# Performance work log

Measured on AMD Instinct MI355X. Metric: run time of the kernel, lower is better.

## Reference

```python
import jax, jax.numpy as jnp
import numpy as np

N_HEADS = 16
THETA = 10000.0


def _rope_cos_sin(seq_len, head_dim):
    # freqs_cis = exp(i * pos * theta^(-2j/d)), shape (seq_len, head_dim//2)
    inv_freq = 1.0 / (THETA ** (np.arange(0, head_dim, 2, dtype=np.float32) / head_dim))
    ang = np.arange(seq_len, dtype=np.float32)[:, None] * inv_freq[None, :]
    return jnp.asarray(np.cos(ang)), jnp.asarray(np.sin(ang))


def _apply_rope(t, cos, sin):
    # t: [B, S, H, hd]; rotate consecutive pairs as complex numbers
    B, S, H, hd = t.shape
    pairs = t.reshape(B, S, H, hd // 2, 2)
    r, i = pairs[..., 0], pairs[..., 1]
    c = cos[None, :, None, :]  # [1, S, 1, hd//2]
    s = sin[None, :, None, :]
    out_r = r * c - i * s
    out_i = r * s + i * c
    return jnp.stack([out_r, out_i], axis=-1).reshape(B, S, H, hd)


def setup_inputs() -> dict:
    key = jax.random.key(0)
    ks = jax.random.split(key, 5)
    B, S, D = 2, 2048, 2048
    scale = 1.0 / np.sqrt(D)
    return {
        "x": jax.random.normal(ks[0], (B, S, D), dtype=jnp.float32),
        "wq": jax.random.normal(ks[1], (D, D), dtype=jnp.float32) * scale,
        "wk": jax.random.normal(ks[2], (D, D), dtype=jnp.float32) * scale,
        "wv": jax.random.normal(ks[3], (D, D), dtype=jnp.float32) * scale,
        "wo": jax.random.normal(ks[4], (D, D), dtype=jnp.float32) * scale,
    }


def reference(x, wq, wk, wv, wo):
    B, S, D = x.shape
    H = N_HEADS
    hd = D // H
    cos, sin = _rope_cos_sin(S, hd)

    xq = (x @ wq.T).reshape(B, S, H, hd)
    xk = (x @ wk.T).reshape(B, S, H, hd)
    xv = (x @ wv.T).reshape(B, S, H, hd)

    xq = _apply_rope(xq, cos, sin)
    xk = _apply_rope(xk, cos, sin)

    # [B, H, S, S] scores, full (non-causal) softmax as in the source
    scores = jnp.einsum("bqhd,bkhd->bhqk", xq, xk) / jnp.sqrt(jnp.float32(hd))
    attn = jax.nn.softmax(scores, axis=-1)
    out = jnp.einsum("bhqk,bkhd->bqhd", attn, xv).reshape(B, S, D)
    return out @ wo.T
```

## Files before the change

kernel.cpp:

```cpp
#include <hip/hip_runtime.h>
#include <hip/hip_bf16.h>
#include <stdint.h>


typedef __attribute__((ext_vector_type(4))) float f32x4;
typedef __attribute__((ext_vector_type(8))) short bf16x8;

typedef __attribute__((address_space(3))) unsigned int lds_u32;
typedef __attribute__((address_space(1))) const unsigned int gbl_u32;

__device__ __forceinline__ void async16(const void* g, void* l) {
  __builtin_amdgcn_global_load_lds((gbl_u32*)g, (lds_u32*)l, 16, 0, 0);
}

__device__ __forceinline__ float bf_to_f(unsigned short u) {
  union { unsigned int i; float f; } v; v.i = ((unsigned int)u) << 16; return v.f;
}
__device__ __forceinline__ unsigned short f_to_bf(float f) {
  union { float f; unsigned int i; } v; v.f = f;
  unsigned int r = v.i + 0x7FFFu + ((v.i >> 16) & 1u);
  return (unsigned short)(r >> 16);
}
__device__ __forceinline__ unsigned int cvt_pk_bf16(float lo, float hi) {
  unsigned int r;
  asm("v_cvt_pk_bf16_f32 %0, %1, %2" : "=v"(r) : "v"(lo), "v"(hi));
  return r;
}

#define B_ 2
#define S_ 2048
#define D_ 2048
#define H_ 16
#define HD_ 128

__global__ __launch_bounds__(256) void conv_all(const float* __restrict__ x,
                                                const float* __restrict__ wq,
                                                const float* __restrict__ wk,
                                                const float* __restrict__ wv,
                                                const float* __restrict__ wo,
                                                unsigned short* __restrict__ xb,
                                                unsigned short* __restrict__ wb) {
  int i = blockIdx.x * 256 + threadIdx.x;
  const float* s;
  unsigned short* d;
  int off;
  if (i < 2097152) {
    s = x; d = xb; off = i;
  } else {
    int j = i - 2097152;
    int t = j >> 20;
    off = j & 1048575;
    s = (t == 0) ? wq : (t == 1) ? wk : (t == 2) ? wv : wo;
    d = wb + (size_t)t * 4194304;
  }
  float4 v = ((const float4*)s)[off];
  uint2 o;
  o.x = (unsigned int)f_to_bf(v.x) | ((unsigned int)f_to_bf(v.y) << 16);
  o.y = (unsigned int)f_to_bf(v.z) | ((unsigned int)f_to_bf(v.w) << 16);
  ((uint2*)d)[off] = o;
}

__global__ __launch_bounds__(256) void rope_table_kernel(float* __restrict__ cosT,
                                                         float* __restrict__ sinT) {
  int i = blockIdx.x * 256 + threadIdx.x;
  int s = i >> 6, j = i & 63;
  float inv = powf(10000.0f, -(float)(2 * j) * (1.0f / 128.0f));
  float ang = (float)s * inv;
  float sv, cv;
  sincosf(ang, &sv, &cv);
  cosT[i] = cv;
  sinT[i] = sv;
}

template <int MODE>
__global__ __launch_bounds__(256, 3) void gemm_bt(const unsigned short* __restrict__ A,
                                                  const unsigned short* __restrict__ Bm,
                                                  unsigned short* __restrict__ Cb,
                                                  float* __restrict__ Cf,
                                                  const float* __restrict__ cosT,
                                                  const float* __restrict__ sinT,
                                                  int M, int N, int K) {
  __shared__ unsigned short sA[128 * 32];
  __shared__ unsigned short sB[128 * 32];
  const int tid = threadIdx.x;
  const int l = tid & 63, wv = tid >> 6;
  const int lane15 = l & 15, lhi = l >> 4;
  const int wm = wv >> 1, wn = wv & 1;
  const int bm = blockIdx.x, bn = blockIdx.y;
  const unsigned short* Ag = A + (size_t)bm * 128 * K;
  const unsigned short* Bg = Bm + (size_t)bn * 128 * K;

  f32x4 acc[4][4];
  const f32x4 zero = {0.f, 0.f, 0.f, 0.f};
#pragma unroll
  for (int i = 0; i < 4; i++)
#pragma unroll
    for (int j = 0; j < 4; j++) acc[i][j] = zero;

  for (int k0 = 0; k0 < K; k0 += 32) {
    __syncthreads();
#pragma unroll
    for (int i = 0; i < 2; i++) {
      int c = i * 256 + tid;
      int row = c >> 2, col = (c & 3) << 3;
      async16(Ag + (size_t)row * K + k0 + col, &sA[c * 8]);
      async16(Bg + (size_t)row * K + k0 + col, &sB[c * 8]);
    }
    __syncthreads();

    bf16x8 af[4], bfr[4];
#pragma unroll
    for (int i = 0; i < 4; i++)
      af[i] = *(const bf16x8*)&sA[(wm * 64 + i * 16 + lane15) * 32 + lhi * 8];
#pragma unroll
    for (int j = 0; j < 4; j++)
      bfr[j] = *(const bf16x8*)&sB[(wn * 64 + j * 16 + lane15) * 32 + lhi * 8];
#pragma unroll
    for (int i = 0; i < 4; i++)
#pragma unroll
      for (int j = 0; j < 4; j++)
        acc[i][j] = __builtin_amdgcn_mfma_f32_16x16x32_bf16(af[i], bfr[j], acc[i][j], 0, 0, 0);
  }

#pragma unroll
  for (int i = 0; i < 4; i++) {
    int m0 = bm * 128 + wm * 64 + i * 16 + lhi * 4;
#pragma unroll
    for (int j = 0; j < 4; j++) {
      int n = bn * 128 + wn * 64 + j * 16 + lane15;
      if constexpr (MODE == 0) {
#pragma unroll
        for (int r = 0; r < 4; r++) Cb[(size_t)(m0 + r) * N + n] = f_to_bf(acc[i][j][r]);
      } else if constexpr (MODE == 1) {
#pragma unroll
        for (int r = 0; r < 4; r++) Cf[(size_t)(m0 + r) * N + n] = acc[i][j][r];
      } else if constexpr (MODE == 2) {
        int s0 = m0 & (S_ - 1);
        int jp = (n & (HD_ - 1)) >> 1;
        int odd = n & 1;
#pragma unroll
        for (int r = 0; r < 4; r++) {
          float own = acc[i][j][r];
          float prt = __shfl_xor(own, 1);
          float c = cosT[(s0 + r) * 64 + jp];
          float sn = sinT[(s0 + r) * 64 + jp];
          float outv = odd ? fmaf(prt, sn, own * c) : own * c - prt * sn;
          Cb[(size_t)(m0 + r) * N + n] = f_to_bf(outv);
        }
      } else {
        int s0 = m0 & (S_ - 1);
        size_t row = (size_t)((m0 >> 11) * D_ + n);
        uint2 st;
        st.x = (unsigned int)f_to_bf(acc[i][j][0]) | ((unsigned int)f_to_bf(acc[i][j][1]) << 16);
        st.y = (unsigned int)f_to_bf(acc[i][j][2]) | ((unsigned int)f_to_bf(acc[i][j][3]) << 16);
        *(uint2*)(Cb + row * S_ + s0) = st;
      }
    }
  }
}

__global__ __launch_bounds__(512, 2) void attn_kernel(const unsigned short* __restrict__ Q,
                                                      const unsigned short* __restrict__ K,
                                                      const unsigned short* __restrict__ Vt,
                                                      unsigned short* __restrict__ ctx,
                                                      const float* __restrict__ cosT,
                                                      const float* __restrict__ sinT) {
  __shared__ unsigned short sK[2][64 * 128];
  __shared__ unsigned short sV[2][128 * 64];
  __shared__ unsigned short sP[8][32 * 72];
  const int tid = threadIdx.x, l = tid & 63, w = tid >> 6;
  const int lane15 = l & 15, lhi = l >> 4;
  const int bh = blockIdx.x * 4 + (blockIdx.y >> 3);
  const int qt = blockIdx.y & 7;
  const int b = bh >> 4, h = bh & 15;
  const int q0 = qt * 256;
  const unsigned short* Kg = K + ((size_t)(b * S_)) * D_ + h * HD_;
  const unsigned short* Vg = Vt + ((size_t)bh * HD_) * S_;
  const float qscale = 0.08838834764831845f * 1.44269504f;
  const float THR = 11.5415603f;

  const unsigned short* gp0;
  const unsigned short* gp1;
  const unsigned short* gp2;
  const unsigned short* gp3;
  unsigned int ldsOff[4];
  int gstride;
  if (w < 4) {
    const unsigned short* t0;
#pragma unroll
    for (int i = 0; i < 4; i++) {
      int row = w * 16 + i * 4 + (l >> 4);
      int colD = (l & 15) << 4;
      int colS = colD ^ ((row & 7) << 4);
      t0 = Kg + (size_t)row * D_ + (colS >> 1);
      if (i == 0) gp0 = t0; else if (i == 1) gp1 = t0; else if (i == 2) gp2 = t0; else gp3 = t0;
      ldsOff[i] = row * 256 + colD;
    }
    gstride = 64 * D_;
  } else {
    const unsigned short* t0;
#pragma unroll
    for (int i = 0; i < 4; i++) {
      int row = (w - 4) * 32 + i * 8 + (l >> 3);
      int colD = (l & 7) << 4;
      int colS = colD ^ ((row & 7) << 4);
      t0 = Vg + (size_t)row * S_ + (colS >> 1);
      if (i == 0) gp0 = t0; else if (i == 1) gp1 = t0; else if (i == 2) gp2 = t0; else gp3 = t0;
      ldsOff[i] = row * 128 + colD;
    }
    gstride = 64;
  }

  bf16x8 qf[2][4];
#pragma unroll
  for (int s = 0; s < 2; s++) {
    int s_q = q0 + w * 32 + s * 16 + lane15;
    const unsigned short* Qrow = Q + ((size_t)(b * S_ + s_q)) * D_ + h * HD_;
#pragma unroll
    for (int kc = 0; kc < 4; kc++) {
      int d0 = kc * 32 + lhi * 8;
      uint4 raw = *(const uint4*)(Qrow + d0);
      float4 cv = *(const float4*)(cosT + (size_t)s_q * 64 + (d0 >> 1));
      float4 sv = *(const float4*)(sinT + (size_t)s_q * 64 + (d0 >> 1));
      unsigned int u[4] = {raw.x, raw.y, raw.z, raw.w};
      float cc[4] = {cv.x, cv.y, cv.z, cv.w};
      float ss[4] = {sv.x, sv.y, sv.z, sv.w};
      unsigned int o[4];
#pragma unroll
      for (int p = 0; p < 4; p++) {
        float re = bf_to_f((unsigned short)(u[p] & 0xffffu));
        float im = bf_to_f((unsigned short)(u[p] >> 16));
        float orr = (re * cc[p] - im * ss[p]) * qscale;
        float oi = (re * ss[p] + im * cc[p]) * qscale;
        o[p] = (unsigned int)f_to_bf(orr) | ((unsigned int)f_to_bf(oi) << 16);
      }
      union { uint4 u4; bf16x8 v; } cvt;
      cvt.u4.x = o[0]; cvt.u4.y = o[1]; cvt.u4.z = o[2]; cvt.u4.w = o[3];
      qf[s][kc] = cvt.v;
    }
  }

  float mrun[2] = {-1e30f, -1e30f}, lrun[2] = {0.f, 0.f};
  const f32x4 zero = {0.f, 0.f, 0.f, 0.f};
  f32x4 oacc[2][8];
#pragma unroll
  for (int s = 0; s < 2; s++)
#pragma unroll
    for (int nf = 0; nf < 8; nf++) oacc[s][nf] = zero;

  {
    char* base = (w < 4) ? (char*)&sK[0][0] : (char*)&sV[0][0];
    async16(gp0, base + ldsOff[0]);
    async16(gp1, base + ldsOff[1]);
    async16(gp2, base + ldsOff[2]);
    async16(gp3, base + ldsOff[3]);
    gp0 += gstride; gp1 += gstride; gp2 += gstride; gp3 += gstride;
  }

  for (int t = 0; t < 32; ++t) {
    const int cur = t & 1;
    __syncthreads();
    if (t < 31) {
      char* base = (w < 4) ? (char*)&sK[cur ^ 1][0] : (char*)&sV[cur ^ 1][0];
      async16(gp0, base + ldsOff[0]);
      async16(gp1, base + ldsOff[1]);
      async16(gp2, base + ldsOff[2]);
      async16(gp3, base + ldsOff[3]);
      gp0 += gstride; gp1 += gstride; gp2 += gstride; gp3 += gstride;
    }
    const unsigned short* sKc = sK[cur];
    const unsigned short* sVc = sV[cur];

    f32x4 sacc[2][4];
#pragma unroll
    for (int s = 0; s < 2; s++)
#pragma unroll
      for (int n = 0; n < 4; n++) sacc[s][n] = zero;
    __builtin_amdgcn_s_setprio(1);
#pragma unroll
    for (int n = 0; n < 4; n++) {
      int row = n * 16 + lane15;
#pragma unroll
      for (int kc = 0; kc < 4; kc++) {
        bf16x8 kf = *(const bf16x8*)((const char*)sKc + row * 256 +
                                     ((kc * 64 + lhi * 16) ^ ((row & 7) << 4)));
        sacc[0][n] = __builtin_amdgcn_mfma_f32_16x16x32_bf16(kf, qf[0][kc], sacc[0][n], 0, 0, 0);
        sacc[1][n] = __builtin_amdgcn_mfma_f32_16x16x32_bf16(kf, qf[1][kc], sacc[1][n], 0, 0, 0);
      }
    }
    __builtin_amdgcn_s_setprio(0);

    float pmax[2];
#pragma unroll
    for (int s = 0; s < 2; s++) {
      float a0 = fmaxf(fmaxf(sacc[s][0][0], sacc[s][0][1]), fmaxf(sacc[s][0][2], sacc[s][0][3]));
      float a1 = fmaxf(fmaxf(sacc[s][1][0], sacc[s][1][1]), fmaxf(sacc[s][1][2], sacc[s][1][3]));
      float a2 = fmaxf(fmaxf(sacc[s][2][0], sacc[s][2][1]), fmaxf(sacc[s][2][2], sacc[s][2][3]));
      float a3 = fmaxf(fmaxf(sacc[s][3][0], sacc[s][3][1]), fmaxf(sacc[s][3][2], sacc[s][3][3]));
      float pm = fmaxf(fmaxf(a0, a1), fmaxf(a2, a3));
      pm = fmaxf(pm, __shfl_xor(pm, 16));
      pm = fmaxf(pm, __shfl_xor(pm, 32));
      pmax[s] = pm;
    }
    if (!__all(fmaxf(pmax[0] - mrun[0], pmax[1] - mrun[1]) <= THR)) {
#pragma unroll
      for (int s = 0; s < 2; s++) {
        float mnew = fmaxf(mrun[s], pmax[s]);
        float alpha = exp2f(mrun[s] - mnew);
        lrun[s] *= alpha;
        float af[4];
#pragma unroll
        for (int r = 0; r < 4; r++) af[r] = __shfl(alpha, lhi * 4 + r);
#pragma unroll
        for (int nf = 0; nf < 8; nf++)
#pragma unroll
          for (int r = 0; r < 4; r++) oacc[s][nf][r] *= af[r];
        mrun[s] = mnew;
      }
    }
#pragma unroll
    for (int s = 0; s < 2; s++) {
      float rs = 0.f;
      float p[4][4];
#pragma unroll
      for (int n = 0; n < 4; n++)
#pragma unroll
        for (int r = 0; r < 4; r++) {
          float pv = exp2f(sacc[s][n][r] - mrun[s]);
          p[n][r] = pv;
          rs += pv;
        }
      rs += __shfl_xor(rs, 16);
      rs += __shfl_xor(rs, 32);
      lrun[s] += rs;
#pragma unroll
      for (int n = 0; n < 4; n++) {
        uint2 st;
        st.x = cvt_pk_bf16(p[n][0], p[n][1]);
        st.y = cvt_pk_bf16(p[n][2], p[n][3]);
        *(uint2*)&sP[w][(s * 16 + lane15) * 72 + n * 16 + lhi * 4] = st;
      }
    }
    asm volatile("s_waitcnt lgkmcnt(0)" ::: "memory");
    __builtin_amdgcn_sched_barrier(0);
    bf16x8 pf[2][2];
#pragma unroll
    for (int s = 0; s < 2; s++)
#pragma unroll
      for (int kc = 0; kc < 2; kc++)
        pf[s][kc] = *(const bf16x8*)&sP[w][(s * 16 + lane15) * 72 + kc * 32 + lhi * 8];

    __builtin_amdgcn_s_setprio(1);
#pragma unroll
    for (int nf = 0; nf < 8; nf++) {
      int row = nf * 16 + lane15;
#pragma unroll
      for (int kc = 0; kc < 2; kc++) {
        bf16x8 vf = *(const bf16x8*)((const char*)sVc + row * 128 +
                                     ((kc * 64 + lhi * 16) ^ ((row & 7) << 4)));
        oacc[0][nf] = __builtin_amdgcn_mfma_f32_16x16x32_bf16(pf[0][kc], vf, oacc[0][nf], 0, 0, 0);
        oacc[1][nf] = __builtin_amdgcn_mfma_f32_16x16x32_bf16(pf[1][kc], vf, oacc[1][nf], 0, 0, 0);
      }
    }
    __builtin_amdgcn_s_setprio(0);
  }

#pragma unroll
  for (int s = 0; s < 2; s++) {
    float inv = 1.0f / lrun[s];
    float invr[4];
#pragma unroll
    for (int r = 0; r < 4; r++) invr[r] = __shfl(inv, lhi * 4 + r);
    unsigned short* Og = ctx + ((size_t)(b * S_ + q0 + w * 32 + s * 16)) * D_ + h * HD_;
#pragma unroll
    for (int r = 0; r < 4; r++) {
      int qrow = lhi * 4 + r;
#pragma unroll
      for (int nf = 0; nf < 8; nf++)
        Og[(size_t)qrow * D_ + nf * 16 + lane15] = f_to_bf(oacc[s][nf][r] * invr[r]);
    }
  }
}

extern "C" void kernel_launch(void* const* d_in, const int* in_sizes, int n_in,
                              void* d_out, int out_size, void* d_ws, size_t ws_size,
                              hipStream_t stream) {
  (void)in_sizes; (void)n_in; (void)out_size; (void)ws_size;
  const float* x = (const float*)d_in[0];
  const float* wq = (const float*)d_in[1];
  const float* wk = (const float*)d_in[2];
  const float* wv = (const float*)d_in[3];
  const float* wo = (const float*)d_in[4];
  float* out = (float*)d_out;

  char* ws = (char*)d_ws;
  const size_t MB = 1024 * 1024;
  unsigned short* xb  = (unsigned short*)(ws + 0 * MB);
  unsigned short* wqb = (unsigned short*)(ws + 16 * MB);
  unsigned short* wkb = (unsigned short*)(ws + 24 * MB);
  unsigned short* wvb = (unsigned short*)(ws + 32 * MB);
  unsigned short* wob = (unsigned short*)(ws + 40 * MB);
  unsigned short* Qb  = (unsigned short*)(ws + 48 * MB);
  unsigned short* Kb  = (unsigned short*)(ws + 64 * MB);
  unsigned short* Vtb = (unsigned short*)(ws + 80 * MB);
  float* cosT = (float*)(ws + 96 * MB);
  float* sinT = (float*)(ws + 96 * MB + 524288);
  unsigned short* ctxb = xb;

  const int M = B_ * S_;

  conv_all<<<24576, 256, 0, stream>>>(x, wq, wk, wv, wo, xb, wqb);
  rope_table_kernel<<<512, 256, 0, stream>>>(cosT, sinT);

  dim3 ggrid(M / 128, D_ / 128);
  gemm_bt<0><<<ggrid, 256, 0, stream>>>(xb, wqb, Qb, nullptr, nullptr, nullptr, M, D_, D_);
  gemm_bt<2><<<ggrid, 256, 0, stream>>>(xb, wkb, Kb, nullptr, cosT, sinT, M, D_, D_);
  gemm_bt<3><<<ggrid, 256, 0, stream>>>(xb, wvb, Vtb, nullptr, nullptr, nullptr, M, D_, D_);

  attn_kernel<<<dim3(8, 32), 512, 0, stream>>>(Qb, Kb, Vtb, ctxb, cosT, sinT);

  gemm_bt<1><<<ggrid, 256, 0, stream>>>(ctxb, wob, nullptr, out, nullptr, nullptr, M, D_, D_);
}
```

Before: 314.6 us.

## Shrink attention blocks to 4 waves, swap P via permlane, remap grid per XCD

The attention kernel now runs 256-thread blocks of 128 query rows each, launched as a 1D grid of 512 blocks. Block indices are mapped so that the blocks sharing one batch-head land on the same XCD, which should improve L2 reuse of K and V. Every wave now loads both K and V tiles, where before half the waves loaded each. The P matrix goes from the C-fragment layout to the A-operand layout with v_permlane32/16_swap in registers rather than a round trip through LDS, which removes the sP buffer, its LDS traffic and the waitcnt. In exchange each block issues more loads per wave and there are twice as many blocks.

Result: no change. 320.7 us (+1.9%).

```diff
diff --git a/kernel.cpp b/kernel.cpp
--- a/kernel.cpp
+++ b/kernel.cpp
@@ -159,7 +159,7 @@
   }
 }
 
-__global__ __launch_bounds__(512, 2) void attn_kernel(const unsigned short* __restrict__ Q,
+__global__ __launch_bounds__(256, 2) void attn_kernel(const unsigned short* __restrict__ Q,
                                                       const unsigned short* __restrict__ K,
                                                       const unsigned short* __restrict__ Vt,
                                                       unsigned short* __restrict__ ctx,
@@ -167,48 +167,34 @@
                                                       const float* __restrict__ sinT) {
   __shared__ unsigned short sK[2][64 * 128];
   __shared__ unsigned short sV[2][128 * 64];
-  __shared__ unsigned short sP[8][32 * 72];
   const int tid = threadIdx.x, l = tid & 63, w = tid >> 6;
   const int lane15 = l & 15, lhi = l >> 4;
-  const int bh = blockIdx.x * 4 + (blockIdx.y >> 3);
-  const int qt = blockIdx.y & 7;
+  const int wg = blockIdx.x;
+  const int xcd = wg & 7, rest = wg >> 3;
+  const int bh = xcd * 4 + (rest >> 4);
+  const int qt = rest & 15;
   const int b = bh >> 4, h = bh & 15;
-  const int q0 = qt * 256;
+  const int q0 = qt * 128;
   const unsigned short* Kg = K + ((size_t)(b * S_)) * D_ + h * HD_;
   const unsigned short* Vg = Vt + ((size_t)bh * HD_) * S_;
   const float qscale = 0.08838834764831845f * 1.44269504f;
   const float THR = 11.5415603f;
 
-  const unsigned short* gp0;
-  const unsigned short* gp1;
-  const unsigned short* gp2;
-  const unsigned short* gp3;
-  unsigned int ldsOff[4];
-  int gstride;
-  if (w < 4) {
-    const unsigned short* t0;
-#pragma unroll
-    for (int i = 0; i < 4; i++) {
-      int row = w * 16 + i * 4 + (l >> 4);
-      int colD = (l & 15) << 4;
-      int colS = colD ^ ((row & 7) << 4);
-      t0 = Kg + (size_t)row * D_ + (colS >> 1);
-      if (i == 0) gp0 = t0; else if (i == 1) gp1 = t0; else if (i == 2) gp2 = t0; else gp3 = t0;
-      ldsOff[i] = row * 256 + colD;
-    }
-    gstride = 64 * D_;
-  } else {
-    const unsigned short* t0;
-#pragma unroll
-    for (int i = 0; i < 4; i++) {
-      int row = (w - 4) * 32 + i * 8 + (l >> 3);
-      int colD = (l & 7) << 4;
-      int colS = colD ^ ((row & 7) << 4);
-      t0 = Vg + (size_t)row * S_ + (colS >> 1);
-      if (i == 0) gp0 = t0; else if (i == 1) gp1 = t0; else if (i == 2) gp2 = t0; else gp3 = t0;
-      ldsOff[i] = row * 128 + colD;
-    }
-    gstride = 64;
+  const unsigned short* gpK[4];
+  const unsigned short* gpV[4];
+  unsigned int offK[4], offV[4];
+#pragma unroll
+  for (int i = 0; i < 4; i++) {
+    int rowK = w * 16 + i * 4 + (l >> 4);
+    int cDK = (l & 15) << 4;
+    int cSK = cDK ^ ((rowK & 7) << 4);
+    gpK[i] = Kg + (size_t)rowK * D_ + (cSK >> 1);
+    offK[i] = rowK * 256 + cDK;
+    int rowV = w * 32 + i * 8 + (l >> 3);
+    int cDV = (l & 7) << 4;
+    int cSV = cDV ^ ((rowV & 7) << 4);
+    gpV[i] = Vg + (size_t)rowV * S_ + (cSV >> 1);
+    offV[i] = rowV * 128 + cDV;
   }
 
   bf16x8 qf[2][4];
@@ -248,25 +234,31 @@
 #pragma unroll
     for (int nf = 0; nf < 8; nf++) oacc[s][nf] = zero;
 
-  {
-    char* base = (w < 4) ? (char*)&sK[0][0] : (char*)&sV[0][0];
-    async16(gp0, base + ldsOff[0]);
-    async16(gp1, base + ldsOff[1]);
-    async16(gp2, base + ldsOff[2]);
-    async16(gp3, base + ldsOff[3]);
-    gp0 += gstride; gp1 += gstride; gp2 += gstride; gp3 += gstride;
+#pragma unroll
+  for (int i = 0; i < 4; i++) {
+    async16(gpK[i], (char*)&sK[0][0] + offK[i]);
+    gpK[i] += 64 * D_;
+  }
+#pragma unroll
+  for (int i = 0; i < 4; i++) {
+    async16(gpV[i], (char*)&sV[0][0] + offV[i]);
+    gpV[i] += 64;
   }
 
   for (int t = 0; t < 32; ++t) {
     const int cur = t & 1;
     __syncthreads();
     if (t < 31) {
-      char* base = (w < 4) ? (char*)&sK[cur ^ 1][0] : (char*)&sV[cur ^ 1][0];
-      async16(gp0, base + ldsOff[0]);
-      async16(gp1, base + ldsOff[1]);
-      async16(gp2, base + ldsOff[2]);
-      async16(gp3, base + ldsOff[3]);
-      gp0 += gstride; gp1 += gstride; gp2 += gstride; gp3 += gstride;
+#pragma unroll
+      for (int i = 0; i < 4; i++) {
+        async16(gpK[i], (char*)&sK[cur ^ 1][0] + offK[i]);
+        gpK[i] += 64 * D_;
+      }
+#pragma unroll
+      for (int i = 0; i < 4; i++) {
+        async16(gpV[i], (char*)&sV[cur ^ 1][0] + offV[i]);
+        gpV[i] += 64;
+      }
     }
     const unsigned short* sKc = sK[cur];
     const unsigned short* sVc = sV[cur];
@@ -318,6 +310,7 @@
         mrun[s] = mnew;
       }
     }
+    bf16x8 paS[2][2];
 #pragma unroll
     for (int s = 0; s < 2; s++) {
       float rs = 0.f;
@@ -333,22 +326,25 @@
       rs += __shfl_xor(rs, 16);
       rs += __shfl_xor(rs, 32);
       lrun[s] += rs;
+      unsigned int wlo[4], whi[4];
 #pragma unroll
       for (int n = 0; n < 4; n++) {
-        uint2 st;
-        st.x = cvt_pk_bf16(p[n][0], p[n][1]);
-        st.y = cvt_pk_bf16(p[n][2], p[n][3]);
-        *(uint2*)&sP[w][(s * 16 + lane15) * 72 + n * 16 + lhi * 4] = st;
-      }
-    }
-    asm volatile("s_waitcnt lgkmcnt(0)" ::: "memory");
-    __builtin_amdgcn_sched_barrier(0);
-    bf16x8 pf[2][2];
-#pragma unroll
-    for (int s = 0; s < 2; s++)
-#pragma unroll
-      for (int kc = 0; kc < 2; kc++)
-        pf[s][kc] = *(const bf16x8*)&sP[w][(s * 16 + lane15) * 72 + kc * 32 + lhi * 8];
+        wlo[n] = cvt_pk_bf16(p[n][0], p[n][1]);
+        whi[n] = cvt_pk_bf16(p[n][2], p[n][3]);
+      }
+#pragma unroll
+      for (int kc = 0; kc < 2; kc++) {
+        unsigned int A = wlo[2 * kc], Bw = whi[2 * kc];
+        unsigned int C = wlo[2 * kc + 1], Dw = whi[2 * kc + 1];
+        asm("v_permlane32_swap_b32 %0, %1" : "+v"(A), "+v"(C));
+        asm("v_permlane16_swap_b32 %0, %1" : "+v"(A), "+v"(C));
+        asm("v_permlane32_swap_b32 %0, %1" : "+v"(Bw), "+v"(Dw));
+        asm("v_permlane16_swap_b32 %0, %1" : "+v"(Bw), "+v"(Dw));
+        union { uint4 u4; bf16x8 v; } pk;
+        pk.u4.x = A; pk.u4.y = Bw; pk.u4.z = C; pk.u4.w = Dw;
+        paS[s][kc] = pk.v;
+      }
+    }
 
     __builtin_amdgcn_s_setprio(1);
 #pragma unroll
@@ -358,8 +354,8 @@
       for (int kc = 0; kc < 2; kc++) {
         bf16x8 vf = *(const bf16x8*)((const char*)sVc + row * 128 +
                                      ((kc * 64 + lhi * 16) ^ ((row & 7) << 4)));
-        oacc[0][nf] = __builtin_amdgcn_mfma_f32_16x16x32_bf16(pf[0][kc], vf, oacc[0][nf], 0, 0, 0);
-        oacc[1][nf] = __builtin_amdgcn_mfma_f32_16x16x32_bf16(pf[1][kc], vf, oacc[1][nf], 0, 0, 0);
+        oacc[0][nf] = __builtin_amdgcn_mfma_f32_16x16x32_bf16(paS[0][kc], vf, oacc[0][nf], 0, 0, 0);
+        oacc[1][nf] = __builtin_amdgcn_mfma_f32_16x16x32_bf16(paS[1][kc], vf, oacc[1][nf], 0, 0, 0);
       }
     }
     __builtin_amdgcn_s_setprio(0);
@@ -417,7 +413,7 @@
   gemm_bt<2><<<ggrid, 256, 0, stream>>>(xb, wkb, Kb, nullptr, cosT, sinT, M, D_, D_);
   gemm_bt<3><<<ggrid, 256, 0, stream>>>(xb, wvb, Vtb, nullptr, nullptr, nullptr, M, D_, D_);
 
-  attn_kernel<<<dim3(8, 32), 512, 0, stream>>>(Qb, Kb, Vtb, ctxb, cosT, sinT);
+  attn_kernel<<<512, 256, 0, stream>>>(Qb, Kb, Vtb, ctxb, cosT, sinT);
 
   gemm_bt<1><<<ggrid, 256, 0, stream>>>(ctxb, wob, nullptr, out, nullptr, nullptr, M, D_, D_);
 }
```

## Fuse Q/K/V projections into one GEMM launch and keep P in registers

Applied to the files above, without the earlier changes.

Replaces the three separate projection GEMM launches with a single launch over a 48-column-tile grid that reads the contiguous wq/wk/wv bf16 buffer and picks the epilogue (plain, RoPE, transposed V) by sector. This cuts launch overhead and tail effects and fills the GPU better with one larger grid. Separately, the attention kernel no longer round-trips the softmax probabilities through LDS. It uses v_permlane32/16_swap to reshape the accumulator layout into MFMA A-operand fragments directly, which removes the LDS stores, waits and reloads, at the cost of relying on a correct lane permutation.

After: 292.6 us. -7.0%, faster.

```diff
diff --git a/kernel.cpp b/kernel.cpp
--- a/kernel.cpp
+++ b/kernel.cpp
@@ -72,16 +72,97 @@
   sinT[i] = sv;
 }
 
-template <int MODE>
-__global__ __launch_bounds__(256, 3) void gemm_bt(const unsigned short* __restrict__ A,
-                                                  const unsigned short* __restrict__ Bm,
-                                                  unsigned short* __restrict__ Cb,
-                                                  float* __restrict__ Cf,
-                                                  const float* __restrict__ cosT,
-                                                  const float* __restrict__ sinT,
-                                                  int M, int N, int K) {
+__global__ __launch_bounds__(256, 3) void qkv_gemm(const unsigned short* __restrict__ A,
+                                                   const unsigned short* __restrict__ W,
+                                                   unsigned short* __restrict__ Qb,
+                                                   unsigned short* __restrict__ Kb,
+                                                   unsigned short* __restrict__ Vtb,
+                                                   const float* __restrict__ cosT,
+                                                   const float* __restrict__ sinT) {
   __shared__ unsigned short sA[128 * 32];
   __shared__ unsigned short sB[128 * 32];
+  const int K = 2048, N = 2048;
+  const int tid = threadIdx.x;
+  const int l = tid & 63, wv = tid >> 6;
+  const int lane15 = l & 15, lhi = l >> 4;
+  const int wm = wv >> 1, wn = wv & 1;
+  const int bm = blockIdx.x, bn = blockIdx.y;
+  const int sector = bn >> 4, bnl = bn & 15;
+  const unsigned short* Ag = A + (size_t)bm * 128 * K;
+  const unsigned short* Bg = W + (size_t)bn * 128 * K;
+
+  f32x4 acc[4][4];
+  const f32x4 zero = {0.f, 0.f, 0.f, 0.f};
+#pragma unroll
+  for (int i = 0; i < 4; i++)
+#pragma unroll
+    for (int j = 0; j < 4; j++) acc[i][j] = zero;
+
+  for (int k0 = 0; k0 < K; k0 += 32) {
+    __syncthreads();
+#pragma unroll
+    for (int i = 0; i < 2; i++) {
+      int c = i * 256 + tid;
+      int row = c >> 2, col = (c & 3) << 3;
+      async16(Ag + (size_t)row * K + k0 + col, &sA[c * 8]);
+      async16(Bg + (size_t)row * K + k0 + col, &sB[c * 8]);
+    }
+    __syncthreads();
+
+    bf16x8 af[4], bfr[4];
+#pragma unroll
+    for (int i = 0; i < 4; i++)
+      af[i] = *(const bf16x8*)&sA[(wm * 64 + i * 16 + lane15) * 32 + lhi * 8];
+#pragma unroll
+    for (int j = 0; j < 4; j++)
+      bfr[j] = *(const bf16x8*)&sB[(wn * 64 + j * 16 + lane15) * 32 + lhi * 8];
+#pragma unroll
+    for (int i = 0; i < 4; i++)
+#pragma unroll
+      for (int j = 0; j < 4; j++)
+        acc[i][j] = __builtin_amdgcn_mfma_f32_16x16x32_bf16(af[i], bfr[j], acc[i][j], 0, 0, 0);
+  }
+
+#pragma unroll
+  for (int i = 0; i < 4; i++) {
+    int m0 = bm * 128 + wm * 64 + i * 16 + lhi * 4;
+#pragma unroll
+    for (int j = 0; j < 4; j++) {
+      int n = bnl * 128 + wn * 64 + j * 16 + lane15;
+      if (sector == 0) {
+#pragma unroll
+        for (int r = 0; r < 4; r++) Qb[(size_t)(m0 + r) * N + n] = f_to_bf(acc[i][j][r]);
+      } else if (sector == 1) {
+        int s0 = m0 & (S_ - 1);
+        int jp = (n & (HD_ - 1)) >> 1;
+        int odd = n & 1;
+#pragma unroll
+        for (int r = 0; r < 4; r++) {
+          float own = acc[i][j][r];
+          float prt = __shfl_xor(own, 1);
+          float c = cosT[(s0 + r) * 64 + jp];
+          float sn = sinT[(s0 + r) * 64 + jp];
+          float outv = odd ? fmaf(prt, sn, own * c) : own * c - prt * sn;
+          Kb[(size_t)(m0 + r) * N + n] = f_to_bf(outv);
+        }
+      } else {
+        int s0 = m0 & (S_ - 1);
+        size_t row = (size_t)((m0 >> 11) * D_ + n);
+        uint2 st;
+        st.x = (unsigned int)f_to_bf(acc[i][j][0]) | ((unsigned int)f_to_bf(acc[i][j][1]) << 16);
+        st.y = (unsigned int)f_to_bf(acc[i][j][2]) | ((unsigned int)f_to_bf(acc[i][j][3]) << 16);
+        *(uint2*)(Vtb + row * S_ + s0) = st;
+      }
+    }
+  }
+}
+
+__global__ __launch_bounds__(256, 3) void gemm_out(const unsigned short* __restrict__ A,
+                                                   const unsigned short* __restrict__ Bm,
+                                                   float* __restrict__ Cf) {
+  __shared__ unsigned short sA[128 * 32];
+  __shared__ unsigned short sB[128 * 32];
+  const int K = 2048, N = 2048;
   const int tid = threadIdx.x;
   const int l = tid & 63, wv = tid >> 6;
   const int lane15 = l & 15, lhi = l >> 4;
@@ -128,33 +209,8 @@
 #pragma unroll
     for (int j = 0; j < 4; j++) {
       int n = bn * 128 + wn * 64 + j * 16 + lane15;
-      if constexpr (MODE == 0) {
-#pragma unroll
-        for (int r = 0; r < 4; r++) Cb[(size_t)(m0 + r) * N + n] = f_to_bf(acc[i][j][r]);
-      } else if constexpr (MODE == 1) {
-#pragma unroll
-        for (int r = 0; r < 4; r++) Cf[(size_t)(m0 + r) * N + n] = acc[i][j][r];
-      } else if constexpr (MODE == 2) {
-        int s0 = m0 & (S_ - 1);
-        int jp = (n & (HD_ - 1)) >> 1;
-        int odd = n & 1;
-#pragma unroll
-        for (int r = 0; r < 4; r++) {
-          float own = acc[i][j][r];
-          float prt = __shfl_xor(own, 1);
-          float c = cosT[(s0 + r) * 64 + jp];
-          float sn = sinT[(s0 + r) * 64 + jp];
-          float outv = odd ? fmaf(prt, sn, own * c) : own * c - prt * sn;
-          Cb[(size_t)(m0 + r) * N + n] = f_to_bf(outv);
-        }
-      } else {
-        int s0 = m0 & (S_ - 1);
-        size_t row = (size_t)((m0 >> 11) * D_ + n);
-        uint2 st;
-        st.x = (unsigned int)f_to_bf(acc[i][j][0]) | ((unsigned int)f_to_bf(acc[i][j][1]) << 16);
-        st.y = (unsigned int)f_to_bf(acc[i][j][2]) | ((unsigned int)f_to_bf(acc[i][j][3]) << 16);
-        *(uint2*)(Cb + row * S_ + s0) = st;
-      }
+#pragma unroll
+      for (int r = 0; r < 4; r++) Cf[(size_t)(m0 + r) * N + n] = acc[i][j][r];
     }
   }
 }
@@ -167,7 +223,6 @@
                                                       const float* __restrict__ sinT) {
   __shared__ unsigned short sK[2][64 * 128];
   __shared__ unsigned short sV[2][128 * 64];
-  __shared__ unsigned short sP[8][32 * 72];
   const int tid = threadIdx.x, l = tid & 63, w = tid >> 6;
   const int lane15 = l & 15, lhi = l >> 4;
   const int bh = blockIdx.x * 4 + (blockIdx.y >> 3);
@@ -318,6 +373,7 @@
         mrun[s] = mnew;
       }
     }
+    bf16x8 paS[2][2];
 #pragma unroll
     for (int s = 0; s < 2; s++) {
       float rs = 0.f;
@@ -333,22 +389,25 @@
       rs += __shfl_xor(rs, 16);
       rs += __shfl_xor(rs, 32);
       lrun[s] += rs;
+      unsigned int wlo[4], whi[4];
 #pragma unroll
       for (int n = 0; n < 4; n++) {
-        uint2 st;
-        st.x = cvt_pk_bf16(p[n][0], p[n][1]);
-        st.y = cvt_pk_bf16(p[n][2], p[n][3]);
-        *(uint2*)&sP[w][(s * 16 + lane15) * 72 + n * 16 + lhi * 4] = st;
-      }
-    }
-    asm volatile("s_waitcnt lgkmcnt(0)" ::: "memory");
-    __builtin_amdgcn_sched_barrier(0);
-    bf16x8 pf[2][2];
-#pragma unroll
-    for (int s = 0; s < 2; s++)
-#pragma unroll
-      for (int kc = 0; kc < 2; kc++)
-        pf[s][kc] = *(const bf16x8*)&sP[w][(s * 16 + lane15) * 72 + kc * 32 + lhi * 8];
+        wlo[n] = cvt_pk_bf16(p[n][0], p[n][1]);
+        whi[n] = cvt_pk_bf16(p[n][2], p[n][3]);
+      }
+#pragma unroll
+      for (int kc = 0; kc < 2; kc++) {
+        unsigned int A = wlo[2 * kc], Bw = whi[2 * kc];
+        unsigned int C = wlo[2 * kc + 1], Dw = whi[2 * kc + 1];
+        asm("v_permlane32_swap_b32 %0, %1" : "+v"(A), "+v"(C));
+        asm("v_permlane16_swap_b32 %0, %1" : "+v"(A), "+v"(C));
+        asm("v_permlane32_swap_b32 %0, %1" : "+v"(Bw), "+v"(Dw));
+        asm("v_permlane16_swap_b32 %0, %1" : "+v"(Bw), "+v"(Dw));
+        union { uint4 u4; bf16x8 v; } pk;
+        pk.u4.x = A; pk.u4.y = Bw; pk.u4.z = C; pk.u4.w = Dw;
+        paS[s][kc] = pk.v;
+      }
+    }
 
     __builtin_amdgcn_s_setprio(1);
 #pragma unroll
@@ -358,8 +417,8 @@
       for (int kc = 0; kc < 2; kc++) {
         bf16x8 vf = *(const bf16x8*)((const char*)sVc + row * 128 +
                                      ((kc * 64 + lhi * 16) ^ ((row & 7) << 4)));
-        oacc[0][nf] = __builtin_amdgcn_mfma_f32_16x16x32_bf16(pf[0][kc], vf, oacc[0][nf], 0, 0, 0);
-        oacc[1][nf] = __builtin_amdgcn_mfma_f32_16x16x32_bf16(pf[1][kc], vf, oacc[1][nf], 0, 0, 0);
+        oacc[0][nf] = __builtin_amdgcn_mfma_f32_16x16x32_bf16(paS[0][kc], vf, oacc[0][nf], 0, 0, 0);
+        oacc[1][nf] = __builtin_amdgcn_mfma_f32_16x16x32_bf16(paS[1][kc], vf, oacc[1][nf], 0, 0, 0);
       }
     }
     __builtin_amdgcn_s_setprio(0);
@@ -397,8 +456,6 @@
   const size_t MB = 1024 * 1024;
   unsigned short* xb  = (unsigned short*)(ws + 0 * MB);
   unsigned short* wqb = (unsigned short*)(ws + 16 * MB);
-  unsigned short* wkb = (unsigned short*)(ws + 24 * MB);
-  unsigned short* wvb = (unsigned short*)(ws + 32 * MB);
   unsigned short* wob = (unsigned short*)(ws + 40 * MB);
   unsigned short* Qb  = (unsigned short*)(ws + 48 * MB);
   unsigned short* Kb  = (unsigned short*)(ws + 64 * MB);
@@ -412,12 +469,9 @@
   conv_all<<<24576, 256, 0, stream>>>(x, wq, wk, wv, wo, xb, wqb);
   rope_table_kernel<<<512, 256, 0, stream>>>(cosT, sinT);
 
-  dim3 ggrid(M / 128, D_ / 128);
-  gemm_bt<0><<<ggrid, 256, 0, stream>>>(xb, wqb, Qb, nullptr, nullptr, nullptr, M, D_, D_);
-  gemm_bt<2><<<ggrid, 256, 0, stream>>>(xb, wkb, Kb, nullptr, cosT, sinT, M, D_, D_);
-  gemm_bt<3><<<ggrid, 256, 0, stream>>>(xb, wvb, Vtb, nullptr, nullptr, nullptr, M, D_, D_);
+  qkv_gemm<<<dim3(M / 128, 48), 256, 0, stream>>>(xb, wqb, Qb, Kb, Vtb, cosT, sinT);
 
   attn_kernel<<<dim3(8, 32), 512, 0, stream>>>(Qb, Kb, Vtb, ctxb, cosT, sinT);
 
-  gemm_bt<1><<<ggrid, 256, 0, stream>>>(ctxb, wob, nullptr, out, nullptr, nullptr, M, D_, D_);
-}
+  gemm_out<<<dim3(M / 128, D_ / 128), 256, 0, stream>>>(ctxb, wob, out);
+}
```
